# Kernel tuning notes

Measured on AMD Instinct MI355X. Metric: run time of the kernel, lower is better.

The kernel has to match this reference:

```python
import jax, jax.numpy as jnp
import numpy as np

N = 50000   # nodes
E = 800000  # edges (avg degree 16)
D = 128     # in = hidden = out channels (residual path active)
EPS = 1e-5  # BatchNorm eps


def setup_inputs() -> dict:
    key = jax.random.key(0)
    ks = jax.random.split(key, 24)
    sc = 1.0 / np.sqrt(D)
    inp = {
        "x": jax.random.normal(ks[0], (N, D), jnp.float32),
        "W1": jax.random.normal(ks[1], (D, D), jnp.float32) * sc,
        "b1": jnp.zeros((D,), jnp.float32),
        "g1": 1.0 + 0.1 * jax.random.normal(ks[2], (D,), jnp.float32),
        "be1": 0.1 * jax.random.normal(ks[3], (D,), jnp.float32),
        "m1": 0.1 * jax.random.normal(ks[4], (D,), jnp.float32),
        "v1": 0.5 + jax.random.uniform(ks[5], (D,), jnp.float32),
        "W2": jax.random.normal(ks[6], (D, D), jnp.float32) * sc,
        "b2": jnp.zeros((D,), jnp.float32),
        "g2": 1.0 + 0.1 * jax.random.normal(ks[7], (D,), jnp.float32),
        "be2": 0.1 * jax.random.normal(ks[8], (D,), jnp.float32),
        "m2": 0.1 * jax.random.normal(ks[9], (D,), jnp.float32),
        "v2": 0.5 + jax.random.uniform(ks[10], (D,), jnp.float32),
        "W3": jax.random.normal(ks[11], (D, D), jnp.float32) * sc,
        "b3": jnp.zeros((D,), jnp.float32),
        "src": jax.random.randint(ks[12], (E,), 0, N, jnp.int32),
        "dst": jax.random.randint(ks[13], (E,), 0, N, jnp.int32),
    }
    return inp


def _gcn_conv(x, W, b, src, dst):
    # PyG GCNConv: add self-loops, symmetric D^{-1/2}(A+I)D^{-1/2} normalization.
    h = x @ W                                              # [N, C]
    deg = jax.ops.segment_sum(jnp.ones((E,), x.dtype), dst, num_segments=N) + 1.0
    dinv = jax.lax.rsqrt(deg)                              # [N]
    coef = dinv[src] * dinv[dst]                           # [E]
    agg = jax.ops.segment_sum(h[src] * coef[:, None], dst, num_segments=N)
    agg = agg + h * (dinv * dinv)[:, None]                 # self-loop term
    return agg + b


def _bn(x, g, be, m, v):
    # eval-mode BatchNorm1d with running stats
    return (x - m) * jax.lax.rsqrt(v + EPS) * g + be


def reference(x, W1, b1, g1, be1, m1, v1, W2, b2, g2, be2, m2, v2, W3, b3, src, dst):
    x_res = x
    h = jax.nn.relu(_bn(_gcn_conv(x, W1, b1, src, dst), g1, be1, m1, v1))
    h = jax.nn.relu(_bn(_gcn_conv(h, W2, b2, src, dst), g2, be2, m2, v2))
    h = _gcn_conv(h, W3, b3, src, dst)
    return h + x_res  # in_channels == out_channels -> residual active
```

## Files before the change

### kernel.cpp

```cpp
#include <hip/hip_runtime.h>
#include <hip/hip_bf16.h>


#define GCN_N 50000
#define GCN_E 800000
#define GCN_D 128

__global__ __launch_bounds__(256) void zero_kernel(int* __restrict__ p, int n) {
    int i = blockIdx.x * blockDim.x + threadIdx.x;
    if (i < n) p[i] = 0;
}

__global__ __launch_bounds__(256) void hist_kernel(const int* __restrict__ dst,
                                                   int* __restrict__ cnt, int nE) {
    int e = blockIdx.x * blockDim.x + threadIdx.x;
    if (e < nE) atomicAdd(&cnt[dst[e]], 1);
}

__global__ __launch_bounds__(256) void block_reduce(const int* __restrict__ cnt,
                                                    int* __restrict__ bsum, int n) {
    int tid = threadIdx.x, lane = tid & 63, wid = tid >> 6;
    int i0 = blockIdx.x * 1024 + tid * 4;
    int s = 0;
    #pragma unroll
    for (int q = 0; q < 4; ++q)
        if (i0 + q < n) s += cnt[i0 + q];
    #pragma unroll
    for (int off = 32; off >= 1; off >>= 1) s += __shfl_xor(s, off);
    __shared__ int ws[4];
    if (lane == 0) ws[wid] = s;
    __syncthreads();
    if (tid == 0) bsum[blockIdx.x] = ws[0] + ws[1] + ws[2] + ws[3];
}

__global__ void scan_bsums(const int* __restrict__ bsum, int* __restrict__ boff,
                           int nb, int* __restrict__ row_last) {
    int lane = threadIdx.x;
    int v = (lane < nb) ? bsum[lane] : 0;
    int sc = v;
    #pragma unroll
    for (int off = 1; off < 64; off <<= 1) {
        int t = __shfl_up(sc, off);
        if (lane >= off) sc += t;
    }
    if (lane < nb) boff[lane] = sc - v;
    if (lane == 63) *row_last = sc;
}

__global__ __launch_bounds__(256) void scan_apply(const int* __restrict__ cnt_in,
                                                  const int* __restrict__ boff,
                                                  int* __restrict__ row_ptr,
                                                  float* __restrict__ dinv,
                                                  int* __restrict__ cnt_zero, int n) {
    __shared__ int wsum[4];
    int tid = threadIdx.x, lane = tid & 63, wid = tid >> 6;
    int i0 = blockIdx.x * 1024 + tid * 4;
    int a0 = 0, a1 = 0, a2 = 0, a3 = 0;
    if (i0 + 0 < n) a0 = cnt_in[i0 + 0];
    if (i0 + 1 < n) a1 = cnt_in[i0 + 1];
    if (i0 + 2 < n) a2 = cnt_in[i0 + 2];
    if (i0 + 3 < n) a3 = cnt_in[i0 + 3];
    int tsum = a0 + a1 + a2 + a3;
    int sc = tsum;
    #pragma unroll
    for (int off = 1; off < 64; off <<= 1) {
        int t = __shfl_up(sc, off);
        if (lane >= off) sc += t;
    }
    if (lane == 63) wsum[wid] = sc;
    __syncthreads();
    int woff = 0;
    #pragma unroll
    for (int w = 0; w < 4; ++w)
        if (w < wid) woff += wsum[w];
    int excl = boff[blockIdx.x] + woff + (sc - tsum);
    if (i0 + 0 < n) { row_ptr[i0 + 0] = excl;                dinv[i0 + 0] = rsqrtf((float)a0 + 1.f); cnt_zero[i0 + 0] = 0; }
    if (i0 + 1 < n) { row_ptr[i0 + 1] = excl + a0;           dinv[i0 + 1] = rsqrtf((float)a1 + 1.f); cnt_zero[i0 + 1] = 0; }
    if (i0 + 2 < n) { row_ptr[i0 + 2] = excl + a0 + a1;      dinv[i0 + 2] = rsqrtf((float)a2 + 1.f); cnt_zero[i0 + 2] = 0; }
    if (i0 + 3 < n) { row_ptr[i0 + 3] = excl + a0 + a1 + a2; dinv[i0 + 3] = rsqrtf((float)a3 + 1.f); cnt_zero[i0 + 3] = 0; }
}

__global__ __launch_bounds__(256) void fill_kernel(const int* __restrict__ src,
                                                   const int* __restrict__ dst,
                                                   const int* __restrict__ row_ptr,
                                                   int* __restrict__ cur,
                                                   const float* __restrict__ dinv,
                                                   int2* __restrict__ emeta, int nE) {
    int e = blockIdx.x * blockDim.x + threadIdx.x;
    if (e >= nE) return;
    int d = dst[e], s = src[e];
    int pos = row_ptr[d] + atomicAdd(&cur[d], 1);
    emeta[pos] = make_int2(s, __float_as_int(dinv[s] * dinv[d]));
}

__global__ void prep_kernel(const float* __restrict__ b, const float* __restrict__ g,
                            const float* __restrict__ be, const float* __restrict__ m,
                            const float* __restrict__ v, float* __restrict__ scale,
                            float* __restrict__ shift) {
    int c = threadIdx.x;
    float s = g[c] * rsqrtf(v[c] + 1e-5f);
    scale[c] = s;
    shift[c] = (b[c] - m[c]) * s + be[c];
}

__global__ __launch_bounds__(256) void mm_kernel(const float* __restrict__ A,
                                                 const float* __restrict__ W,
                                                 float* __restrict__ H, int n) {
    __shared__ float As[64][68];
    __shared__ float Bs[64][132];
    int tid = threadIdx.x;
    int tx = tid & 15;
    int ty = tid >> 4;
    int row0 = blockIdx.x * 64;
    float acc[4][8] = {};

    for (int k0 = 0; k0 < 128; k0 += 64) {
        int ac = (tid & 15) * 4;
        int ar = tid >> 4;
        #pragma unroll
        for (int rr = 0; rr < 4; ++rr) {
            int r = ar + rr * 16;
            int gr = row0 + r;
            float4 v = make_float4(0.f, 0.f, 0.f, 0.f);
            if (gr < n) v = *(const float4*)&A[(size_t)gr * GCN_D + k0 + ac];
            *(float4*)&As[r][ac] = v;
        }
        int bc = (tid & 31) * 4;
        int br = tid >> 5;
        #pragma unroll
        for (int rr = 0; rr < 8; ++rr) {
            int r = br + rr * 8;
            float4 v = *(const float4*)&W[(size_t)(k0 + r) * GCN_D + bc];
            *(float4*)&Bs[r][bc] = v;
        }
        __syncthreads();
        #pragma unroll
        for (int kk = 0; kk < 64; ++kk) {
            float a[4];
            #pragma unroll
            for (int m = 0; m < 4; ++m) a[m] = As[ty * 4 + m][kk];
            float4 b0 = *(const float4*)&Bs[kk][tx * 8];
            float4 b1 = *(const float4*)&Bs[kk][tx * 8 + 4];
            float b[8] = {b0.x, b0.y, b0.z, b0.w, b1.x, b1.y, b1.z, b1.w};
            #pragma unroll
            for (int m = 0; m < 4; ++m)
                #pragma unroll
                for (int q = 0; q < 8; ++q) acc[m][q] += a[m] * b[q];
        }
        __syncthreads();
    }
    #pragma unroll
    for (int m = 0; m < 4; ++m) {
        int gr = row0 + ty * 4 + m;
        if (gr < n) {
            *(float4*)&H[(size_t)gr * GCN_D + tx * 8] =
                make_float4(acc[m][0], acc[m][1], acc[m][2], acc[m][3]);
            *(float4*)&H[(size_t)gr * GCN_D + tx * 8 + 4] =
                make_float4(acc[m][4], acc[m][5], acc[m][6], acc[m][7]);
        }
    }
}

template <int FINAL>
__global__ __launch_bounds__(256) void agg_kernel(const float* __restrict__ h,
                                                  const int* __restrict__ row_ptr,
                                                  const int2* __restrict__ emeta,
                                                  const float* __restrict__ dinv,
                                                  const float* __restrict__ scale,
                                                  const float* __restrict__ shift,
                                                  const float* __restrict__ xres,
                                                  float* __restrict__ out, int n) {
    int wid = threadIdx.x >> 6, lane = threadIdx.x & 63;
    int node = blockIdx.x * 4 + wid;
    if (node >= n) return;
    int c0 = lane * 2;
    float di = dinv[node];
    float dd = di * di;
    float2 self = *(const float2*)&h[(size_t)node * GCN_D + c0];
    float ax = self.x * dd, ay = self.y * dd;
    float bx = 0.f, by = 0.f;
    int j = row_ptr[node], end = row_ptr[node + 1];
    for (; j + 3 < end; j += 4) {
        int2 m0 = emeta[j + 0];
        int2 m1 = emeta[j + 1];
        int2 m2 = emeta[j + 2];
        int2 m3 = emeta[j + 3];
        float2 h0 = *(const float2*)&h[(size_t)m0.x * GCN_D + c0];
        float2 h1 = *(const float2*)&h[(size_t)m1.x * GCN_D + c0];
        float2 h2 = *(const float2*)&h[(size_t)m2.x * GCN_D + c0];
        float2 h3 = *(const float2*)&h[(size_t)m3.x * GCN_D + c0];
        float w0 = __int_as_float(m0.y), w1 = __int_as_float(m1.y);
        float w2 = __int_as_float(m2.y), w3 = __int_as_float(m3.y);
        ax += h0.x * w0 + h1.x * w1;
        ay += h0.y * w0 + h1.y * w1;
        bx += h2.x * w2 + h3.x * w3;
        by += h2.y * w2 + h3.y * w3;
    }
    for (; j < end; ++j) {
        int2 m = emeta[j];
        float w = __int_as_float(m.y);
        float2 hh = *(const float2*)&h[(size_t)m.x * GCN_D + c0];
        ax += hh.x * w;
        ay += hh.y * w;
    }
    float accx = ax + bx, accy = ay + by;
    float2 o;
    if (FINAL) {
        float2 b = *(const float2*)&scale[c0];
        float2 xr = *(const float2*)&xres[(size_t)node * GCN_D + c0];
        o.x = accx + b.x + xr.x;
        o.y = accy + b.y + xr.y;
    } else {
        float2 sc = *(const float2*)&scale[c0];
        float2 sh = *(const float2*)&shift[c0];
        o.x = fmaxf(accx * sc.x + sh.x, 0.f);
        o.y = fmaxf(accy * sc.y + sh.y, 0.f);
    }
    *(float2*)&out[(size_t)node * GCN_D + c0] = o;
}

extern "C" void kernel_launch(void* const* d_in, const int* in_sizes, int n_in,
                              void* d_out, int out_size, void* d_ws, size_t ws_size,
                              hipStream_t stream) {
    (void)in_sizes; (void)n_in; (void)out_size; (void)ws_size;
    const int N = GCN_N, E = GCN_E, D = GCN_D;

    const float* x   = (const float*)d_in[0];
    const float* W1  = (const float*)d_in[1];
    const float* b1  = (const float*)d_in[2];
    const float* g1  = (const float*)d_in[3];
    const float* be1 = (const float*)d_in[4];
    const float* m1  = (const float*)d_in[5];
    const float* v1  = (const float*)d_in[6];
    const float* W2  = (const float*)d_in[7];
    const float* b2  = (const float*)d_in[8];
    const float* g2  = (const float*)d_in[9];
    const float* be2 = (const float*)d_in[10];
    const float* m2  = (const float*)d_in[11];
    const float* v2  = (const float*)d_in[12];
    const float* W3  = (const float*)d_in[13];
    const float* b3  = (const float*)d_in[14];
    const int* src   = (const int*)d_in[15];
    const int* dst   = (const int*)d_in[16];
    float* out = (float*)d_out;

    float* h      = (float*)d_ws;
    float* act    = h + (size_t)N * D;
    float* dinv   = act + (size_t)N * D;
    int* cnt      = (int*)(dinv + N);
    int* row_ptr  = cnt + N;
    int2* emeta   = (int2*)(row_ptr + N + 2);
    float* scale1 = (float*)(emeta + E);
    float* shift1 = scale1 + D;
    float* scale2 = shift1 + D;
    float* shift2 = scale2 + D;
    int* bsum     = (int*)(shift2 + D);
    int* boff     = bsum + 64;

    const int NB = (N + 1023) / 1024;

    zero_kernel<<<(N + 255) / 256, 256, 0, stream>>>(cnt, N);
    hist_kernel<<<(E + 255) / 256, 256, 0, stream>>>(dst, cnt, E);
    block_reduce<<<NB, 256, 0, stream>>>(cnt, bsum, N);
    scan_bsums<<<1, 64, 0, stream>>>(bsum, boff, NB, &row_ptr[N]);
    scan_apply<<<NB, 256, 0, stream>>>(cnt, boff, row_ptr, dinv, cnt, N);
    fill_kernel<<<(E + 255) / 256, 256, 0, stream>>>(src, dst, row_ptr, cnt, dinv,
                                                     emeta, E);
    prep_kernel<<<1, D, 0, stream>>>(b1, g1, be1, m1, v1, scale1, shift1);
    prep_kernel<<<1, D, 0, stream>>>(b2, g2, be2, m2, v2, scale2, shift2);

    int mm_grid = (N + 63) / 64;
    int agg_grid = (N + 3) / 4;

    mm_kernel<<<mm_grid, 256, 0, stream>>>(x, W1, h, N);
    agg_kernel<0><<<agg_grid, 256, 0, stream>>>(h, row_ptr, emeta, dinv,
                                                scale1, shift1, nullptr, act, N);
    mm_kernel<<<mm_grid, 256, 0, stream>>>(act, W2, h, N);
    agg_kernel<0><<<agg_grid, 256, 0, stream>>>(h, row_ptr, emeta, dinv,
                                                scale2, shift2, nullptr, act, N);
    mm_kernel<<<mm_grid, 256, 0, stream>>>(act, W3, h, N);
    agg_kernel<1><<<agg_grid, 256, 0, stream>>>(h, row_ptr, emeta, dinv,
                                                b3, nullptr, x, out, N);
}
```

Before: 473.3 us.

## Pre-scale features by dinv and aggregate over 16-channel column slices

The matmul epilogue now multiplies each row by dinv and writes H into a sliced layout of eight 16-channel slabs, so edge metadata shrinks to source indices only and per-edge weights disappear (the coefficient is factored as dinv[dst]*dinv[src]). Aggregation launches eight blocks per node group, one per slice. In each block a wave handles one node with four edges in flight per step across 16 channels, then reduces with shuffles. The goal is to cut edge metadata traffic and keep each slice's gather working set small enough for cache. The cost is more blocks, re-reading row_ptr and esrc once per slice, and 64-byte gathers in place of full-row accesses.

```diff
diff --git a/kernel.cpp b/kernel.cpp
--- a/kernel.cpp
+++ b/kernel.cpp
@@ -5,6 +5,7 @@
 #define GCN_N 50000
 #define GCN_E 800000
 #define GCN_D 128
+#define SLW 16
 
 __global__ __launch_bounds__(256) void zero_kernel(int* __restrict__ p, int n) {
     int i = blockIdx.x * blockDim.x + threadIdx.x;
@@ -84,13 +85,12 @@
                                                    const int* __restrict__ dst,
                                                    const int* __restrict__ row_ptr,
                                                    int* __restrict__ cur,
-                                                   const float* __restrict__ dinv,
-                                                   int2* __restrict__ emeta, int nE) {
+                                                   int* __restrict__ esrc, int nE) {
     int e = blockIdx.x * blockDim.x + threadIdx.x;
     if (e >= nE) return;
-    int d = dst[e], s = src[e];
+    int d = dst[e];
     int pos = row_ptr[d] + atomicAdd(&cur[d], 1);
-    emeta[pos] = make_int2(s, __float_as_int(dinv[s] * dinv[d]));
+    esrc[pos] = src[e];
 }
 
 __global__ void prep_kernel(const float* __restrict__ b, const float* __restrict__ g,
@@ -105,7 +105,8 @@
 
 __global__ __launch_bounds__(256) void mm_kernel(const float* __restrict__ A,
                                                  const float* __restrict__ W,
-                                                 float* __restrict__ H, int n) {
+                                                 const float* __restrict__ dinv,
+                                                 float* __restrict__ h8, int n) {
     __shared__ float As[64][68];
     __shared__ float Bs[64][132];
     int tid = threadIdx.x;
@@ -149,74 +150,63 @@
         }
         __syncthreads();
     }
+    int slice = tx >> 1;
+    int off = (tx & 1) * 8;
     #pragma unroll
     for (int m = 0; m < 4; ++m) {
         int gr = row0 + ty * 4 + m;
         if (gr < n) {
-            *(float4*)&H[(size_t)gr * GCN_D + tx * 8] =
-                make_float4(acc[m][0], acc[m][1], acc[m][2], acc[m][3]);
-            *(float4*)&H[(size_t)gr * GCN_D + tx * 8 + 4] =
-                make_float4(acc[m][4], acc[m][5], acc[m][6], acc[m][7]);
+            float dv = dinv[gr];
+            float* p = h8 + ((size_t)slice * n + gr) * SLW + off;
+            *(float4*)&p[0] = make_float4(acc[m][0] * dv, acc[m][1] * dv,
+                                          acc[m][2] * dv, acc[m][3] * dv);
+            *(float4*)&p[4] = make_float4(acc[m][4] * dv, acc[m][5] * dv,
+                                          acc[m][6] * dv, acc[m][7] * dv);
         }
     }
 }
 
 template <int FINAL>
-__global__ __launch_bounds__(256) void agg_kernel(const float* __restrict__ h,
+__global__ __launch_bounds__(256) void agg_kernel(const float* __restrict__ h8,
                                                   const int* __restrict__ row_ptr,
-                                                  const int2* __restrict__ emeta,
+                                                  const int* __restrict__ esrc,
                                                   const float* __restrict__ dinv,
                                                   const float* __restrict__ scale,
                                                   const float* __restrict__ shift,
                                                   const float* __restrict__ xres,
                                                   float* __restrict__ out, int n) {
+    int slice = blockIdx.x & 7;
+    int bnode = blockIdx.x >> 3;
     int wid = threadIdx.x >> 6, lane = threadIdx.x & 63;
-    int node = blockIdx.x * 4 + wid;
+    int node = bnode * 4 + wid;
     if (node >= n) return;
-    int c0 = lane * 2;
-    float di = dinv[node];
-    float dd = di * di;
-    float2 self = *(const float2*)&h[(size_t)node * GCN_D + c0];
-    float ax = self.x * dd, ay = self.y * dd;
-    float bx = 0.f, by = 0.f;
-    int j = row_ptr[node], end = row_ptr[node + 1];
-    for (; j + 3 < end; j += 4) {
-        int2 m0 = emeta[j + 0];
-        int2 m1 = emeta[j + 1];
-        int2 m2 = emeta[j + 2];
-        int2 m3 = emeta[j + 3];
-        float2 h0 = *(const float2*)&h[(size_t)m0.x * GCN_D + c0];
-        float2 h1 = *(const float2*)&h[(size_t)m1.x * GCN_D + c0];
-        float2 h2 = *(const float2*)&h[(size_t)m2.x * GCN_D + c0];
-        float2 h3 = *(const float2*)&h[(size_t)m3.x * GCN_D + c0];
-        float w0 = __int_as_float(m0.y), w1 = __int_as_float(m1.y);
-        float w2 = __int_as_float(m2.y), w3 = __int_as_float(m3.y);
-        ax += h0.x * w0 + h1.x * w1;
-        ay += h0.y * w0 + h1.y * w1;
-        bx += h2.x * w2 + h3.x * w3;
-        by += h2.y * w2 + h3.y * w3;
-    }
-    for (; j < end; ++j) {
-        int2 m = emeta[j];
-        float w = __int_as_float(m.y);
-        float2 hh = *(const float2*)&h[(size_t)m.x * GCN_D + c0];
-        ax += hh.x * w;
-        ay += hh.y * w;
-    }
-    float accx = ax + bx, accy = ay + by;
-    float2 o;
-    if (FINAL) {
-        float2 b = *(const float2*)&scale[c0];
-        float2 xr = *(const float2*)&xres[(size_t)node * GCN_D + c0];
-        o.x = accx + b.x + xr.x;
-        o.y = accy + b.y + xr.y;
-    } else {
-        float2 sc = *(const float2*)&scale[c0];
-        float2 sh = *(const float2*)&shift[c0];
-        o.x = fmaxf(accx * sc.x + sh.x, 0.f);
-        o.y = fmaxf(accy * sc.y + sh.y, 0.f);
-    }
-    *(float2*)&out[(size_t)node * GCN_D + c0] = o;
+    int c = lane & 15, e4 = lane >> 4;
+    const float* __restrict__ hs = h8 + (size_t)slice * n * SLW;
+    int start = row_ptr[node], end = row_ptr[node + 1];
+    float acc = (e4 == 0) ? hs[(size_t)node * SLW + c] : 0.f;
+    int j = start;
+    for (; j + 8 <= end; j += 8) {
+        float v0 = hs[(size_t)esrc[j + e4] * SLW + c];
+        float v1 = hs[(size_t)esrc[j + 4 + e4] * SLW + c];
+        acc += v0;
+        acc += v1;
+    }
+    int j0 = j + e4, j1 = j + 4 + e4;
+    if (j0 < end) acc += hs[(size_t)esrc[j0] * SLW + c];
+    if (j1 < end) acc += hs[(size_t)esrc[j1] * SLW + c];
+    acc += __shfl_xor(acc, 16);
+    acc += __shfl_xor(acc, 32);
+    if (lane < 16) {
+        int ch = slice * SLW + c;
+        float v = acc * dinv[node];
+        float o;
+        if (FINAL) {
+            o = v + scale[ch] + xres[(size_t)node * GCN_D + ch];
+        } else {
+            o = fmaxf(v * scale[ch] + shift[ch], 0.f);
+        }
+        out[(size_t)node * GCN_D + ch] = o;
+    }
 }
 
 extern "C" void kernel_launch(void* const* d_in, const int* in_sizes, int n_in,
@@ -244,13 +234,13 @@
     const int* dst   = (const int*)d_in[16];
     float* out = (float*)d_out;
 
-    float* h      = (float*)d_ws;
-    float* act    = h + (size_t)N * D;
+    float* h8     = (float*)d_ws;
+    float* act    = h8 + (size_t)N * D;
     float* dinv   = act + (size_t)N * D;
     int* cnt      = (int*)(dinv + N);
     int* row_ptr  = cnt + N;
-    int2* emeta   = (int2*)(row_ptr + N + 2);
-    float* scale1 = (float*)(emeta + E);
+    int* esrc     = row_ptr + (N + 2);
+    float* scale1 = (float*)(esrc + E);
     float* shift1 = scale1 + D;
     float* scale2 = shift1 + D;
     float* shift2 = scale2 + D;
@@ -264,21 +254,20 @@
     block_reduce<<<NB, 256, 0, stream>>>(cnt, bsum, N);
     scan_bsums<<<1, 64, 0, stream>>>(bsum, boff, NB, &row_ptr[N]);
     scan_apply<<<NB, 256, 0, stream>>>(cnt, boff, row_ptr, dinv, cnt, N);
-    fill_kernel<<<(E + 255) / 256, 256, 0, stream>>>(src, dst, row_ptr, cnt, dinv,
-                                                     emeta, E);
+    fill_kernel<<<(E + 255) / 256, 256, 0, stream>>>(src, dst, row_ptr, cnt, esrc, E);
     prep_kernel<<<1, D, 0, stream>>>(b1, g1, be1, m1, v1, scale1, shift1);
     prep_kernel<<<1, D, 0, stream>>>(b2, g2, be2, m2, v2, scale2, shift2);
 
     int mm_grid = (N + 63) / 64;
-    int agg_grid = (N + 3) / 4;
-
-    mm_kernel<<<mm_grid, 256, 0, stream>>>(x, W1, h, N);
-    agg_kernel<0><<<agg_grid, 256, 0, stream>>>(h, row_ptr, emeta, dinv,
+    int agg_grid = ((N + 3) / 4) * 8;
+
+    mm_kernel<<<mm_grid, 256, 0, stream>>>(x, W1, dinv, h8, N);
+    agg_kernel<0><<<agg_grid, 256, 0, stream>>>(h8, row_ptr, esrc, dinv,
                                                 scale1, shift1, nullptr, act, N);
-    mm_kernel<<<mm_grid, 256, 0, stream>>>(act, W2, h, N);
-    agg_kernel<0><<<agg_grid, 256, 0, stream>>>(h, row_ptr, emeta, dinv,
+    mm_kernel<<<mm_grid, 256, 0, stream>>>(act, W2, dinv, h8, N);
+    agg_kernel<0><<<agg_grid, 256, 0, stream>>>(h8, row_ptr, esrc, dinv,
                                                 scale2, shift2, nullptr, act, N);
-    mm_kernel<<<mm_grid, 256, 0, stream>>>(act, W3, h, N);
-    agg_kernel<1><<<agg_grid, 256, 0, stream>>>(h, row_ptr, emeta, dinv,
+    mm_kernel<<<mm_grid, 256, 0, stream>>>(act, W3, dinv, h8, N);
+    agg_kernel<1><<<agg_grid, 256, 0, stream>>>(h8, row_ptr, esrc, dinv,
                                                 b3, nullptr, x, out, N);
 }
```

New measurement: 700.2 us. 47.9% more time.
